# Kernel optimization log

Hardware: AMD Instinct MI355X
Metric: run time of the kernel (lower is better)

The kernel has to match this reference:

```python
import jax, jax.numpy as jnp
import numpy as np

NUM_HEADS = 8
KERNEL = 7  # square 7x7 neighborhood, stride=1, dilation=1, non-causal


def _window_starts(length, kernel):
    # NATTEN window: centered at query, clamped so the full window stays in-bounds
    return jnp.clip(jnp.arange(length) - kernel // 2, 0, length - kernel)


def setup_inputs() -> dict:
    key = jax.random.key(0)
    k1, k2, k3, k4, k5 = jax.random.split(key, 5)
    B, H, W, C = 2, 48, 48, 512
    x = jax.random.normal(k1, (B, H, W, C), dtype=jnp.float32)
    qkv_w = jax.random.normal(k2, (3 * C, C), dtype=jnp.float32) * 0.02
    qkv_b = jax.random.normal(k3, (3 * C,), dtype=jnp.float32) * 0.02
    proj_w = jax.random.normal(k4, (C, C), dtype=jnp.float32) * 0.02
    proj_b = jax.random.normal(k5, (C,), dtype=jnp.float32) * 0.02
    return {"x": x, "qkv_w": qkv_w, "qkv_b": qkv_b, "proj_w": proj_w, "proj_b": proj_b}


def reference(x, qkv_w, qkv_b, proj_w, proj_b):
    B, H, W, C = x.shape
    nh, hd, kk = NUM_HEADS, C // NUM_HEADS, KERNEL
    scale = hd ** -0.5

    # QKV projection: [B,H,W,3,nh,hd]
    qkv = (x @ qkv_w.T + qkv_b).reshape(B, H, W, 3, nh, hd)
    q = qkv[..., 0, :, :] * scale  # [B,H,W,nh,hd]
    k = qkv[..., 1, :, :]
    v = qkv[..., 2, :, :]

    # Neighbor index maps (clamped sliding windows)
    ridx = _window_starts(H, kk)[:, None] + jnp.arange(kk)[None, :]  # [H,kk]
    cidx = _window_starts(W, kk)[:, None] + jnp.arange(kk)[None, :]  # [W,kk]

    # Gather key/value windows: [B,H,kk,W,kk,nh,hd]
    kw = k[:, ridx][:, :, :, cidx]
    vw = v[:, ridx][:, :, :, cidx]

    # Attention over the 7x7 window per query
    attn = jnp.einsum('bijhd,bipjqhd->bhijpq', q, kw)  # [B,nh,H,W,kk,kk]
    attn = jax.nn.softmax(attn.reshape(B, nh, H, W, kk * kk), axis=-1)
    attn = attn.reshape(B, nh, H, W, kk, kk)
    out = jnp.einsum('bhijpq,bipjqhd->bijhd', attn, vw)  # [B,H,W,nh,hd]

    out = out.reshape(B, H, W, C)
    return out @ proj_w.T + proj_b
```

## Files before the change

kernel.cpp:

```cpp
#include <hip/hip_runtime.h>

typedef __bf16 bf16_t;
typedef __bf16 bf16x8 __attribute__((ext_vector_type(8)));
typedef __bf16 bf16x4 __attribute__((ext_vector_type(4)));
typedef float  f32x4  __attribute__((ext_vector_type(4)));

static constexpr int B_   = 2;
static constexpr int H_   = 48;
static constexpr int W_   = 48;
static constexpr int C_   = 512;
static constexpr int NH_  = 8;
static constexpr int HD_  = 64;
static constexpr int KW_  = 7;
static constexpr int ROWS_ = B_ * H_ * W_;
static constexpr int QKVN_ = 3 * C_;

#define GLDS16(g, l) __builtin_amdgcn_global_load_lds(                       \
    (const __attribute__((address_space(1))) void*)(g),                      \
    (__attribute__((address_space(3))) void*)(l), 16, 0, 0)

__global__ __launch_bounds__(256)
void convert_kernel(const float* __restrict__ x,  const float* __restrict__ qw,
                    const float* __restrict__ pw,
                    bf16_t* __restrict__ xb, bf16_t* __restrict__ qwb,
                    bf16_t* __restrict__ pwb)
{
    constexpr int NX = ROWS_ * C_;
    constexpr int NQ = QKVN_ * C_;
    constexpr int NP = C_ * C_;
    const int idx = (blockIdx.x * 256 + threadIdx.x) * 4;
    if (idx >= NX + NQ + NP) return;
    const float* src; bf16_t* dst; int off;
    if (idx < NX)           { src = x;  dst = xb;  off = idx; }
    else if (idx < NX + NQ) { src = qw; dst = qwb; off = idx - NX; }
    else                    { src = pw; dst = pwb; off = idx - NX - NQ; }
    const float4 v = *reinterpret_cast<const float4*>(src + off);
    bf16x4 o;
    o[0] = (bf16_t)v.x; o[1] = (bf16_t)v.y; o[2] = (bf16_t)v.z; o[3] = (bf16_t)v.w;
    *reinterpret_cast<bf16x4*>(dst + off) = o;
}

template<int BM, int BN, int WMT, int WNT, int KTILE, typename OutT>
__global__ __launch_bounds__(256)
void gemm_bt(const bf16_t* __restrict__ A, const bf16_t* __restrict__ Wt,
             const float* __restrict__ bias, OutT* __restrict__ C,
             int M, int N, int K, float scale, int scale_nlim)
{
    constexpr int WCOLS = BN / (WNT * 16);
    constexpr int CPR   = KTILE / 8;
    constexpr int RPI   = 64 / CPR;
    constexpr int KSN   = KTILE / 32;
    __shared__ bf16_t Al[BM * KTILE];
    __shared__ bf16_t Bl[BN * KTILE];

    const int tid  = threadIdx.x;
    const int wave = tid >> 6;
    const int lane = tid & 63;
    const int bm = blockIdx.y * BM;
    const int bn = blockIdx.x * BN;
    const int wm = (wave / WCOLS) * (WMT * 16);
    const int wn = (wave % WCOLS) * (WNT * 16);
    const int n15 = lane & 15, q4 = lane >> 4, x7 = lane & 7;
    const int srow = lane / CPR;
    const int schunk = lane % CPR;

    f32x4 acc[WMT][WNT] = {};

    for (int k0 = 0; k0 < K; k0 += KTILE) {
        __syncthreads();
        #pragma unroll
        for (int i = wave; i < BM / RPI; i += 4) {
            const int row = i * RPI + srow;
            const int cg = (schunk & ~7) | ((schunk & 7) ^ (row & 7));
            GLDS16(A + (size_t)(bm + row) * K + k0 + cg * 8, Al + i * 512);
        }
        #pragma unroll
        for (int i = wave; i < BN / RPI; i += 4) {
            const int row = i * RPI + srow;
            const int cg = (schunk & ~7) | ((schunk & 7) ^ (row & 7));
            GLDS16(Wt + (size_t)(bn + row) * K + k0 + cg * 8, Bl + i * 512);
        }
        __syncthreads();

        #pragma unroll
        for (int ks = 0; ks < KSN; ++ks) {
            const int g = ks * 4 + q4;
            const int cl = (g & ~7) | ((g & 7) ^ x7);
            bf16x8 a[WMT], b[WNT];
            #pragma unroll
            for (int it = 0; it < WMT; ++it)
                a[it] = *reinterpret_cast<const bf16x8*>(
                    Al + (wm + it * 16 + n15) * KTILE + cl * 8);
            #pragma unroll
            for (int jt = 0; jt < WNT; ++jt)
                b[jt] = *reinterpret_cast<const bf16x8*>(
                    Bl + (wn + jt * 16 + n15) * KTILE + cl * 8);
            #pragma unroll
            for (int it = 0; it < WMT; ++it)
                #pragma unroll
                for (int jt = 0; jt < WNT; ++jt)
                    acc[it][jt] = __builtin_amdgcn_mfma_f32_16x16x32_bf16(
                        a[it], b[jt], acc[it][jt], 0, 0, 0);
        }
    }

    #pragma unroll
    for (int jt = 0; jt < WNT; ++jt) {
        const int col = bn + wn + jt * 16 + n15;
        const float bv = bias[col];
        const float sc = (col < scale_nlim) ? scale : 1.0f;
        #pragma unroll
        for (int it = 0; it < WMT; ++it) {
            const int row0 = bm + wm + it * 16 + q4 * 4;
            #pragma unroll
            for (int r = 0; r < 4; ++r)
                C[(size_t)(row0 + r) * N + col] = (OutT)((acc[it][jt][r] + bv) * sc);
        }
    }
}

static constexpr int WIN  = 196;
static constexpr int WROW = 224;
static constexpr int PST  = 232;
static constexpr int PBYTES = 64 * PST * 2;
static constexpr int VTBYTES = 64 * PST * 2;

__global__ __launch_bounds__(256)
void attn_mfma_kernel(const bf16_t* __restrict__ qkv, bf16_t* __restrict__ attn_out)
{
    int bid = blockIdx.x;
    const int h  = bid & 7;   bid >>= 3;
    const int tj = bid % 6;   bid /= 6;
    const int ti = bid % 6;   bid /= 6;
    const int b  = bid;

    const int tid = threadIdx.x;
    const int wave = tid >> 6;
    const int lane = tid & 63;
    const int n15 = lane & 15, q4 = lane >> 4, x7 = lane & 7;

    const int gi0 = ti * 8, gj0 = tj * 8;
    const int si0 = min(max(gi0 - 3, 0), H_ - 14);
    const int sj0 = min(max(gj0 - 3, 0), W_ - 14);

    __shared__ char smem[PBYTES + VTBYTES + 256];
    bf16_t* Kl   = (bf16_t*)smem;
    bf16_t* P    = (bf16_t*)smem;
    bf16_t* VT   = (bf16_t*)(smem + PBYTES);
    float*  invs = (float*)(smem + PBYTES + VTBYTES);

    for (int i = wave; i < WROW / 8; i += 4) {
        const int wrow = i * 8 + (lane >> 3);
        const int wr = wrow >> 4;
        const int wc = min(wrow & 15, 13);
        const int gp = (b * H_ + si0 + wr) * W_ + sj0 + wc;
        const int cg = (lane & 7) ^ (wrow & 7);
        GLDS16(qkv + (size_t)gp * QKVN_ + C_ + h * HD_ + cg * 8, Kl + i * 512);
    }

    for (int t = tid; t < WIN * 8; t += 256) {
        const int w = t % WIN, c = t / WIN;
        const unsigned wr = ((unsigned)w * 4682u) >> 16;
        const unsigned wc = (unsigned)w - wr * 14u;
        const int gp = (b * H_ + si0 + (int)wr) * W_ + sj0 + (int)wc;
        const bf16x8 v8 = *reinterpret_cast<const bf16x8*>(
            qkv + (size_t)gp * QKVN_ + 2 * C_ + h * HD_ + c * 8);
        const int col = (int)wr * 16 + (int)wc;
        #pragma unroll
        for (int u = 0; u < 8; ++u)
            VT[(c * 8 + u) * PST + col] = v8[u];
    }
    for (int t = tid; t < 64 * 14; t += 256) {
        const int d = t / 14, wr = t % 14;
        VT[d * PST + wr * 16 + 14] = (bf16_t)0.f;
        VT[d * PST + wr * 16 + 15] = (bf16_t)0.f;
    }

    const int pixq = wave * 16 + n15;
    const int gpq = (b * H_ + gi0 + (pixq >> 3)) * W_ + gj0 + (pixq & 7);
    bf16x8 aq[2];
    #pragma unroll
    for (int ks = 0; ks < 2; ++ks)
        aq[ks] = *reinterpret_cast<const bf16x8*>(
            qkv + (size_t)gpq * QKVN_ + h * HD_ + ks * 32 + q4 * 8);

    __syncthreads();

    f32x4 S[14] = {};
    #pragma unroll
    for (int j = 0; j < 14; ++j) {
        #pragma unroll
        for (int ks = 0; ks < 2; ++ks) {
            const int cl = (ks * 4 + q4) ^ x7;
            const bf16x8 bk = *reinterpret_cast<const bf16x8*>(
                Kl + (j * 16 + n15) * 64 + cl * 8);
            S[j] = __builtin_amdgcn_mfma_f32_16x16x32_bf16(aq[ks], bk, S[j], 0, 0, 0);
        }
    }

    int ri[4], cj[4];
    #pragma unroll
    for (int r = 0; r < 4; ++r) {
        const int pix = wave * 16 + q4 * 4 + r;
        const int gi = gi0 + (pix >> 3), gj = gj0 + (pix & 7);
        ri[r] = min(max(gi - 3, 0), H_ - KW_) - si0;
        cj[r] = min(max(gj - 3, 0), W_ - KW_) - sj0;
    }
    #pragma unroll
    for (int j = 0; j < 14; ++j)
        #pragma unroll
        for (int r = 0; r < 4; ++r) {
            const bool valid = ((unsigned)(j - ri[r]) < 7u) &&
                               ((unsigned)(n15 - cj[r]) < 7u);
            S[j][r] = valid ? S[j][r] : -1e30f;
        }

    float mx[4], sm[4];
    #pragma unroll
    for (int r = 0; r < 4; ++r) {
        float m = S[0][r];
        #pragma unroll
        for (int j = 1; j < 14; ++j) m = fmaxf(m, S[j][r]);
        #pragma unroll
        for (int off = 1; off < 16; off <<= 1) m = fmaxf(m, __shfl_xor(m, off));
        mx[r] = m;
    }
    #pragma unroll
    for (int j = 0; j < 14; ++j)
        #pragma unroll
        for (int r = 0; r < 4; ++r)
            S[j][r] = __expf(S[j][r] - mx[r]);
    #pragma unroll
    for (int r = 0; r < 4; ++r) {
        float s = S[0][r];
        #pragma unroll
        for (int j = 1; j < 14; ++j) s += S[j][r];
        #pragma unroll
        for (int off = 1; off < 16; off <<= 1) s += __shfl_xor(s, off);
        sm[r] = s;
    }
    if (n15 == 0) {
        #pragma unroll
        for (int r = 0; r < 4; ++r)
            invs[wave * 16 + q4 * 4 + r] = 1.0f / sm[r];
    }

    __syncthreads();

    #pragma unroll
    for (int j = 0; j < 14; ++j)
        #pragma unroll
        for (int r = 0; r < 4; ++r)
            P[(wave * 16 + q4 * 4 + r) * PST + j * 16 + n15] = (bf16_t)S[j][r];

    __syncthreads();

    f32x4 O[4] = {};
    #pragma unroll
    for (int ks = 0; ks < 7; ++ks) {
        const bf16x8 av = *reinterpret_cast<const bf16x8*>(
            VT + (wave * 16 + n15) * PST + ks * 32 + q4 * 8);
        #pragma unroll
        for (int j = 0; j < 4; ++j) {
            const bf16x8 bp = *reinterpret_cast<const bf16x8*>(
                P + (j * 16 + n15) * PST + ks * 32 + q4 * 8);
            O[j] = __builtin_amdgcn_mfma_f32_16x16x32_bf16(av, bp, O[j], 0, 0, 0);
        }
    }

    #pragma unroll
    for (int j = 0; j < 4; ++j) {
        const int pix = j * 16 + n15;
        const float is = invs[pix];
        const int grow = (b * H_ + gi0 + (pix >> 3)) * W_ + gj0 + (pix & 7);
        const int d0 = wave * 16 + q4 * 4;
        bf16x4 o;
        #pragma unroll
        for (int r = 0; r < 4; ++r) o[r] = (bf16_t)(O[j][r] * is);
        *reinterpret_cast<bf16x4*>(attn_out + (size_t)grow * C_ + h * HD_ + d0) = o;
    }
}

extern "C" void kernel_launch(void* const* d_in, const int* in_sizes, int n_in,
                              void* d_out, int out_size, void* d_ws, size_t ws_size,
                              hipStream_t stream)
{
    const float* x      = (const float*)d_in[0];
    const float* qkv_w  = (const float*)d_in[1];
    const float* qkv_b  = (const float*)d_in[2];
    const float* proj_w = (const float*)d_in[3];
    const float* proj_b = (const float*)d_in[4];
    float* out = (float*)d_out;

    char* w = (char*)d_ws;
    bf16_t* xb    = (bf16_t*)w;  w += (size_t)ROWS_ * C_ * 2;
    bf16_t* qwb   = (bf16_t*)w;  w += (size_t)QKVN_ * C_ * 2;
    bf16_t* pwb   = (bf16_t*)w;  w += (size_t)C_ * C_ * 2;
    bf16_t* qkvb  = (bf16_t*)w;  w += (size_t)ROWS_ * QKVN_ * 2;
    bf16_t* attnb = (bf16_t*)w;

    constexpr int TOT4 = (ROWS_ * C_ + QKVN_ * C_ + C_ * C_) / 4;
    convert_kernel<<<(TOT4 + 255) / 256, 256, 0, stream>>>(x, qkv_w, proj_w, xb, qwb, pwb);

    gemm_bt<128, 128, 4, 4, 64, bf16_t><<<dim3(QKVN_ / 128, ROWS_ / 128), 256, 0, stream>>>(
        xb, qwb, qkv_b, qkvb, ROWS_, QKVN_, C_, 0.125f, C_);

    attn_mfma_kernel<<<dim3(B_ * 6 * 6 * NH_), 256, 0, stream>>>(qkvb, attnb);

    gemm_bt<64, 64, 2, 2, 64, float><<<dim3(C_ / 64, ROWS_ / 64), 256, 0, stream>>>(
        attnb, pwb, proj_b, out, ROWS_, C_, C_, 1.0f, 0);
}
```

Before: 111.3 us.

## Async-load V into swizzled LDS, drop softmax max pass, retile QKV GEMM

V is now copied straight into a swizzled LDS layout with global_load_lds, the same way K is. This replaces the register load plus scalar transposed stores into VT and the zero-padding loop. The PV MFMA operand is instead gathered with eight scalar LDS reads per step. Softmax skips the max-subtraction pass and folds the 1/sum normalization into P before the PV product, which removes the invs buffer. Skipping the max subtraction is only safe when logits stay small. The QKV GEMM tile shrinks from 128x128 to 128x64, doubling the block count for better CU occupancy.

```diff
diff --git a/kernel.cpp b/kernel.cpp
--- a/kernel.cpp
+++ b/kernel.cpp
@@ -119,11 +119,10 @@
     }
 }
 
-static constexpr int WIN  = 196;
 static constexpr int WROW = 224;
 static constexpr int PST  = 232;
-static constexpr int PBYTES = 64 * PST * 2;
-static constexpr int VTBYTES = 64 * PST * 2;
+static constexpr int R1B  = 64 * PST * 2;
+static constexpr int R2B  = WROW * 64 * 2;
 
 __global__ __launch_bounds__(256)
 void attn_mfma_kernel(const bf16_t* __restrict__ qkv, bf16_t* __restrict__ attn_out)
@@ -143,37 +142,21 @@
     const int si0 = min(max(gi0 - 3, 0), H_ - 14);
     const int sj0 = min(max(gj0 - 3, 0), W_ - 14);
 
-    __shared__ char smem[PBYTES + VTBYTES + 256];
-    bf16_t* Kl   = (bf16_t*)smem;
-    bf16_t* P    = (bf16_t*)smem;
-    bf16_t* VT   = (bf16_t*)(smem + PBYTES);
-    float*  invs = (float*)(smem + PBYTES + VTBYTES);
+    __shared__ char smem[R1B + R2B];
+    bf16_t* Kl = (bf16_t*)smem;
+    bf16_t* P  = (bf16_t*)smem;
+    bf16_t* Vl = (bf16_t*)(smem + R1B);
 
     for (int i = wave; i < WROW / 8; i += 4) {
-        const int wrow = i * 8 + (lane >> 3);
-        const int wr = wrow >> 4;
-        const int wc = min(wrow & 15, 13);
+        const int row = i * 8 + (lane >> 3);
+        const int wr = row >> 4;
+        const int wc = min(row & 15, 13);
         const int gp = (b * H_ + si0 + wr) * W_ + sj0 + wc;
-        const int cg = (lane & 7) ^ (wrow & 7);
-        GLDS16(qkv + (size_t)gp * QKVN_ + C_ + h * HD_ + cg * 8, Kl + i * 512);
-    }
-
-    for (int t = tid; t < WIN * 8; t += 256) {
-        const int w = t % WIN, c = t / WIN;
-        const unsigned wr = ((unsigned)w * 4682u) >> 16;
-        const unsigned wc = (unsigned)w - wr * 14u;
-        const int gp = (b * H_ + si0 + (int)wr) * W_ + sj0 + (int)wc;
-        const bf16x8 v8 = *reinterpret_cast<const bf16x8*>(
-            qkv + (size_t)gp * QKVN_ + 2 * C_ + h * HD_ + c * 8);
-        const int col = (int)wr * 16 + (int)wc;
-        #pragma unroll
-        for (int u = 0; u < 8; ++u)
-            VT[(c * 8 + u) * PST + col] = v8[u];
-    }
-    for (int t = tid; t < 64 * 14; t += 256) {
-        const int d = t / 14, wr = t % 14;
-        VT[d * PST + wr * 16 + 14] = (bf16_t)0.f;
-        VT[d * PST + wr * 16 + 15] = (bf16_t)0.f;
+        const bf16_t* gbase = qkv + (size_t)gp * QKVN_ + h * HD_;
+        const int cgk = (lane & 7) ^ (row & 7);
+        GLDS16(gbase + C_ + cgk * 8, Kl + i * 512);
+        const int cgv = (lane & 7) ^ ((row + (row >> 3)) & 7);
+        GLDS16(gbase + 2 * C_ + cgv * 8, Vl + i * 512);
     }
 
     const int pixq = wave * 16 + n15;
@@ -215,21 +198,12 @@
             S[j][r] = valid ? S[j][r] : -1e30f;
         }
 
-    float mx[4], sm[4];
-    #pragma unroll
-    for (int r = 0; r < 4; ++r) {
-        float m = S[0][r];
-        #pragma unroll
-        for (int j = 1; j < 14; ++j) m = fmaxf(m, S[j][r]);
-        #pragma unroll
-        for (int off = 1; off < 16; off <<= 1) m = fmaxf(m, __shfl_xor(m, off));
-        mx[r] = m;
-    }
     #pragma unroll
     for (int j = 0; j < 14; ++j)
         #pragma unroll
         for (int r = 0; r < 4; ++r)
-            S[j][r] = __expf(S[j][r] - mx[r]);
+            S[j][r] = __expf(S[j][r]);
+    float rinv[4];
     #pragma unroll
     for (int r = 0; r < 4; ++r) {
         float s = S[0][r];
@@ -237,46 +211,48 @@
         for (int j = 1; j < 14; ++j) s += S[j][r];
         #pragma unroll
         for (int off = 1; off < 16; off <<= 1) s += __shfl_xor(s, off);
-        sm[r] = s;
-    }
-    if (n15 == 0) {
+        rinv[r] = 1.0f / s;
+    }
+
+    __syncthreads();
+
+    #pragma unroll
+    for (int j = 0; j < 14; ++j)
         #pragma unroll
         for (int r = 0; r < 4; ++r)
-            invs[wave * 16 + q4 * 4 + r] = 1.0f / sm[r];
-    }
+            P[(wave * 16 + q4 * 4 + r) * PST + j * 16 + n15] =
+                (bf16_t)(S[j][r] * rinv[r]);
 
     __syncthreads();
 
-    #pragma unroll
-    for (int j = 0; j < 14; ++j)
-        #pragma unroll
-        for (int r = 0; r < 4; ++r)
-            P[(wave * 16 + q4 * 4 + r) * PST + j * 16 + n15] = (bf16_t)S[j][r];
-
-    __syncthreads();
-
+    const int Xv   = wave * 2 + (n15 >> 3);
+    const int dlow = n15 & 7;
     f32x4 O[4] = {};
     #pragma unroll
     for (int ks = 0; ks < 7; ++ks) {
-        const bf16x8 av = *reinterpret_cast<const bf16x8*>(
-            VT + (wave * 16 + n15) * PST + ks * 32 + q4 * 8);
-        #pragma unroll
-        for (int j = 0; j < 4; ++j) {
+        bf16x8 av;
+        #pragma unroll
+        for (int u = 0; u < 8; ++u) {
+            const int w = ks * 32 + q4 * 8 + u;
+            const int slot = Xv ^ ((w + (w >> 3)) & 7);
+            av[u] = Vl[w * 64 + slot * 8 + dlow];
+        }
+        #pragma unroll
+        for (int j2 = 0; j2 < 4; ++j2) {
             const bf16x8 bp = *reinterpret_cast<const bf16x8*>(
-                P + (j * 16 + n15) * PST + ks * 32 + q4 * 8);
-            O[j] = __builtin_amdgcn_mfma_f32_16x16x32_bf16(av, bp, O[j], 0, 0, 0);
-        }
-    }
-
-    #pragma unroll
-    for (int j = 0; j < 4; ++j) {
-        const int pix = j * 16 + n15;
-        const float is = invs[pix];
+                P + (j2 * 16 + n15) * PST + ks * 32 + q4 * 8);
+            O[j2] = __builtin_amdgcn_mfma_f32_16x16x32_bf16(av, bp, O[j2], 0, 0, 0);
+        }
+    }
+
+    #pragma unroll
+    for (int j2 = 0; j2 < 4; ++j2) {
+        const int pix = j2 * 16 + n15;
         const int grow = (b * H_ + gi0 + (pix >> 3)) * W_ + gj0 + (pix & 7);
         const int d0 = wave * 16 + q4 * 4;
         bf16x4 o;
         #pragma unroll
-        for (int r = 0; r < 4; ++r) o[r] = (bf16_t)(O[j][r] * is);
+        for (int r = 0; r < 4; ++r) o[r] = (bf16_t)(O[j2][r]);
         *reinterpret_cast<bf16x4*>(attn_out + (size_t)grow * C_ + h * HD_ + d0) = o;
     }
 }
@@ -302,7 +278,7 @@
     constexpr int TOT4 = (ROWS_ * C_ + QKVN_ * C_ + C_ * C_) / 4;
     convert_kernel<<<(TOT4 + 255) / 256, 256, 0, stream>>>(x, qkv_w, proj_w, xb, qwb, pwb);
 
-    gemm_bt<128, 128, 4, 4, 64, bf16_t><<<dim3(QKVN_ / 128, ROWS_ / 128), 256, 0, stream>>>(
+    gemm_bt<128, 64, 4, 2, 64, bf16_t><<<dim3(QKVN_ / 64, ROWS_ / 128), 256, 0, stream>>>(
         xb, qwb, qkv_b, qkvb, ROWS_, QKVN_, C_, 0.125f, C_);
 
     attn_mfma_kernel<<<dim3(B_ * 6 * 6 * NH_), 256, 0, stream>>>(qkvb, attnb);
```

Result: faster. 105.9 us (-4.9%).
